# Kernel optimization log

Hardware: AMD Instinct MI355X
Metric: run time of the kernel (lower is better)

The kernel has to match this reference:

```python
import jax, jax.numpy as jnp
import numpy as np


def setup_inputs() -> dict:
    key = jax.random.key(0)
    x = jax.random.normal(key, (8192, 8192), dtype=jnp.float32)
    return {"input_tensor": x}


def reference(input_tensor):
    # (x * 2 + 1) ** 2, single fused elementwise pass
    y = input_tensor * 2.0 + 1.0
    return y * y
```

## Files before the change

kernel.cpp:

```cpp
#include <hip/hip_runtime.h>


__global__ void fused_elemwise_f32(const float* __restrict__ in,
                                   float* __restrict__ out,
                                   long long n4) {
    long long idx = (long long)blockIdx.x * blockDim.x + threadIdx.x;
    long long stride = (long long)gridDim.x * blockDim.x;
    const float4* __restrict__ in4 = (const float4*)in;
    float4* __restrict__ out4 = (float4*)out;
    for (long long i = idx; i < n4; i += stride) {
        float4 v = in4[i];
        float4 r;
        float t0 = fmaf(v.x, 2.0f, 1.0f);
        float t1 = fmaf(v.y, 2.0f, 1.0f);
        float t2 = fmaf(v.z, 2.0f, 1.0f);
        float t3 = fmaf(v.w, 2.0f, 1.0f);
        r.x = t0 * t0;
        r.y = t1 * t1;
        r.z = t2 * t2;
        r.w = t3 * t3;
        out4[i] = r;
    }
}

__global__ void fused_elemwise_f32_tail(const float* __restrict__ in,
                                        float* __restrict__ out,
                                        long long start, long long n) {
    long long i = start + (long long)blockIdx.x * blockDim.x + threadIdx.x;
    if (i < n) {
        float t = fmaf(in[i], 2.0f, 1.0f);
        out[i] = t * t;
    }
}

extern "C" void kernel_launch(void* const* d_in, const int* in_sizes, int n_in,
                              void* d_out, int out_size, void* d_ws, size_t ws_size,
                              hipStream_t stream) {
    const float* in = (const float*)d_in[0];
    float* out = (float*)d_out;
    long long n = (long long)in_sizes[0];
    long long n4 = n / 4;

    const int block = 256;
    int grid = (int)((n4 + block - 1) / block);
    if (grid > 2048) grid = 2048;
    if (grid < 1) grid = 1;

    fused_elemwise_f32<<<grid, block, 0, stream>>>(in, out, n4);

    long long rem_start = n4 * 4;
    if (rem_start < n) {
        long long rem = n - rem_start;
        int tgrid = (int)((rem + block - 1) / block);
        fused_elemwise_f32_tail<<<tgrid, block, 0, stream>>>(in, out, rem_start, n);
    }
}
```

Baseline: 111.1 us.

## Replace grid-stride loop with one-shot blocks, 4 float4 loads per thread, nontemporal access

Drops the capped grid-stride loop in favour of one block per 4096 elements, where each thread issues four independent 16-byte loads before computing. Loads and stores use nontemporal builtins to avoid cache pollution on a pure streaming pass. The goal is more memory requests in flight per thread and less loop and index overhead. The cost is a much larger grid (16384 blocks) and reliance on nontemporal hints behaving well on this hardware.

```diff
diff --git a/kernel.cpp b/kernel.cpp
--- a/kernel.cpp
+++ b/kernel.cpp
@@ -1,31 +1,35 @@
 #include <hip/hip_runtime.h>
 
 
-__global__ void fused_elemwise_f32(const float* __restrict__ in,
-                                   float* __restrict__ out,
-                                   long long n4) {
-    long long idx = (long long)blockIdx.x * blockDim.x + threadIdx.x;
-    long long stride = (long long)gridDim.x * blockDim.x;
-    const float4* __restrict__ in4 = (const float4*)in;
-    float4* __restrict__ out4 = (float4*)out;
-    for (long long i = idx; i < n4; i += stride) {
-        float4 v = in4[i];
-        float4 r;
-        float t0 = fmaf(v.x, 2.0f, 1.0f);
-        float t1 = fmaf(v.y, 2.0f, 1.0f);
-        float t2 = fmaf(v.z, 2.0f, 1.0f);
-        float t3 = fmaf(v.w, 2.0f, 1.0f);
-        r.x = t0 * t0;
-        r.y = t1 * t1;
-        r.z = t2 * t2;
-        r.w = t3 * t3;
-        out4[i] = r;
+typedef float f32x4 __attribute__((ext_vector_type(4)));
+
+__global__ void __launch_bounds__(256) fused_elemwise_x4(
+    const f32x4* __restrict__ in4, f32x4* __restrict__ out4) {
+    long long base = (long long)blockIdx.x * 1024 + threadIdx.x;
+
+    f32x4 a = __builtin_nontemporal_load(&in4[base]);
+    f32x4 b = __builtin_nontemporal_load(&in4[base + 256]);
+    f32x4 c = __builtin_nontemporal_load(&in4[base + 512]);
+    f32x4 d = __builtin_nontemporal_load(&in4[base + 768]);
+
+    #pragma unroll
+    for (int j = 0; j < 4; ++j) {
+        float t;
+        t = fmaf(a[j], 2.0f, 1.0f); a[j] = t * t;
+        t = fmaf(b[j], 2.0f, 1.0f); b[j] = t * t;
+        t = fmaf(c[j], 2.0f, 1.0f); c[j] = t * t;
+        t = fmaf(d[j], 2.0f, 1.0f); d[j] = t * t;
     }
+
+    __builtin_nontemporal_store(a, &out4[base]);
+    __builtin_nontemporal_store(b, &out4[base + 256]);
+    __builtin_nontemporal_store(c, &out4[base + 512]);
+    __builtin_nontemporal_store(d, &out4[base + 768]);
 }
 
-__global__ void fused_elemwise_f32_tail(const float* __restrict__ in,
-                                        float* __restrict__ out,
-                                        long long start, long long n) {
+__global__ void fused_elemwise_tail(const float* __restrict__ in,
+                                    float* __restrict__ out,
+                                    long long start, long long n) {
     long long i = start + (long long)blockIdx.x * blockDim.x + threadIdx.x;
     if (i < n) {
         float t = fmaf(in[i], 2.0f, 1.0f);
@@ -39,19 +43,17 @@
     const float* in = (const float*)d_in[0];
     float* out = (float*)d_out;
     long long n = (long long)in_sizes[0];
-    long long n4 = n / 4;
 
-    const int block = 256;
-    int grid = (int)((n4 + block - 1) / block);
-    if (grid > 2048) grid = 2048;
-    if (grid < 1) grid = 1;
+    long long nblk = n / 4096;
+    if (nblk > 0) {
+        fused_elemwise_x4<<<(int)nblk, 256, 0, stream>>>(
+            (const f32x4*)in, (f32x4*)out);
+    }
 
-    fused_elemwise_f32<<<grid, block, 0, stream>>>(in, out, n4);
-
-    long long rem_start = n4 * 4;
-    if (rem_start < n) {
-        long long rem = n - rem_start;
-        int tgrid = (int)((rem + block - 1) / block);
-        fused_elemwise_f32_tail<<<tgrid, block, 0, stream>>>(in, out, rem_start, n);
+    long long done = nblk * 4096;
+    if (done < n) {
+        long long rem = n - done;
+        int tgrid = (int)((rem + 255) / 256);
+        fused_elemwise_tail<<<tgrid, 256, 0, stream>>>(in, out, done, n);
     }
 }
```

Result: faster. 88.96 us (-19.9%).
